# Kernel tuning notes

Hardware: AMD Instinct MI355X
Metric: run time of the kernel (lower is better)

## Reference

```python
import jax, jax.numpy as jnp
import numpy as np

NHEAD = 8
STRIP = 7  # strip_width (horizontal strips, is_vertical=False)


def setup_inputs() -> dict:
    key = jax.random.key(0)
    k0, k1, k2 = jax.random.split(key, 3)
    B, H, W, C = 2, 112, 112, 256
    x = jax.random.normal(k0, (B, H * W, C), dtype=jnp.float32)
    # torch nn.Linear weights: (out_features, in_features)
    qkv_w = jax.random.normal(k1, (3 * C, C), dtype=jnp.float32) * 0.02
    proj_w = jax.random.normal(k2, (C, C), dtype=jnp.float32) * 0.02
    proj_b = jnp.zeros((C,), dtype=jnp.float32)
    return {"x": x, "qkv_w": qkv_w, "proj_w": proj_w, "proj_b": proj_b,
            "H_feat": 112, "W_feat": 112}


def reference(x, qkv_w, proj_w, proj_b, H_feat, W_feat):
    B, N, C = x.shape
    hd = C // NHEAD
    scale = hd ** -0.5
    n_strips = H_feat // STRIP
    L = STRIP * W_feat  # tokens per horizontal strip
    # window_partition with window (STRIP, W_feat): nwW==1, so a pure reshape
    xs = x.reshape(B * n_strips, L, C)
    # qkv projection (Linear: y = x @ W^T), then split q/k/v and heads
    qkv = jnp.einsum('bnc,dc->bnd', xs, qkv_w)
    qkv = qkv.reshape(B * n_strips, L, 3, NHEAD, hd)
    q, k, v = jnp.moveaxis(qkv, 2, 0)  # each (Bw, L, H, hd)
    attn = jnp.einsum('bnhd,bmhd->bhnm', q * scale, k)
    attn = jax.nn.softmax(attn, axis=-1)
    out = jnp.einsum('bhnm,bmhd->bnhd', attn, v).reshape(B * n_strips, L, C)
    out = jnp.einsum('bnc,dc->bnd', out, proj_w) + proj_b
    # window_reverse is again a pure reshape for horizontal strips
    return out.reshape(B, N, C)
```

## Files before the change

kernel.cpp:

```cpp
#include <hip/hip_runtime.h>
#include <hip/hip_bf16.h>

#define M_ROWS 25088
#define CDIM   256
#define QKVD   768
#define LWIN   784
#define NWINH  256

typedef __attribute__((ext_vector_type(8))) short short8v;
typedef __attribute__((ext_vector_type(4))) float floatx4;

#define CEQ 0.2550660106245232f

static __device__ __forceinline__ float bfs2f(unsigned short s) {
    return __uint_as_float(((unsigned int)s) << 16);
}
static __device__ __forceinline__ unsigned short f2bf(float f) {
    unsigned int x = __float_as_uint(f);
    x += 0x7fffu + ((x >> 16) & 1u);
    return (unsigned short)(x >> 16);
}
static __device__ __forceinline__ unsigned int cvt_pk_bf16(float a, float b) {
    unsigned int r;
    asm("v_cvt_pk_bf16_f32 %0, %1, %2" : "=v"(r) : "v"(a), "v"(b));
    return r;
}
static __device__ __forceinline__ void gld_lds16(const unsigned short* g,
                                                 unsigned short* l) {
    __builtin_amdgcn_global_load_lds(
        (const __attribute__((address_space(1))) unsigned int*)g,
        (__attribute__((address_space(3))) unsigned int*)l, 16, 0, 0);
}

__global__ __launch_bounds__(256) void k_f2bf(
    const float* __restrict__ src, unsigned short* __restrict__ dst, int n8)
{
    const float4* s4 = (const float4*)src;
    uint4* d4 = (uint4*)dst;
    for (int i = blockIdx.x * 256 + threadIdx.x; i < n8;
         i += gridDim.x * 256) {
        float4 a = s4[2 * i], b = s4[2 * i + 1];
        uint4 o;
        o.x = cvt_pk_bf16(a.x, a.y);
        o.y = cvt_pk_bf16(a.z, a.w);
        o.z = cvt_pk_bf16(b.x, b.y);
        o.w = cvt_pk_bf16(b.z, b.w);
        d4[i] = o;
    }
}

template <typename OUT_T, bool BIAS, bool SCALEQ>
__global__ __launch_bounds__(256, 2) void k_gemm_mfma(
    const unsigned short* __restrict__ A,
    const unsigned short* __restrict__ B,
    const float* __restrict__ bias,
    OUT_T* __restrict__ Y, int N)
{
    __shared__ __attribute__((aligned(16))) unsigned short As[128 * 64];
    __shared__ __attribute__((aligned(16))) unsigned short Bs[128 * 64];
    const int t = threadIdx.x;
    const int lane = t & 63, wv = t >> 6;
    const int lq = lane & 15, g = lane >> 4;
    const int wm = wv >> 1, wn = wv & 1;
    const int R0 = blockIdx.y * 128, C0 = blockIdx.x * 128;
    const int lrow = t >> 3, lch = (t & 7) * 8;

    floatx4 acc[4][4];
#pragma unroll
    for (int i = 0; i < 4; ++i)
#pragma unroll
        for (int j = 0; j < 4; ++j) acc[i][j] = (floatx4){0.f, 0.f, 0.f, 0.f};

    for (int kc = 0; kc < 256; kc += 64) {
#pragma unroll
        for (int i = 0; i < 4; ++i) {
            gld_lds16(A + (size_t)(R0 + i * 32 + lrow) * 256 + kc + lch,
                      As + (i * 32 + wv * 8) * 64);
            gld_lds16(B + (size_t)(C0 + i * 32 + lrow) * 256 + kc + lch,
                      Bs + (i * 32 + wv * 8) * 64);
        }
        __syncthreads();
#pragma unroll
        for (int kk = 0; kk < 64; kk += 32) {
            short8v af[4], bf[4];
#pragma unroll
            for (int mi = 0; mi < 4; ++mi)
                af[mi] = *(const short8v*)(As + (wm * 64 + mi * 16 + lq) * 64 +
                                           kk + g * 8);
#pragma unroll
            for (int ni = 0; ni < 4; ++ni)
                bf[ni] = *(const short8v*)(Bs + (wn * 64 + ni * 16 + lq) * 64 +
                                           kk + g * 8);
#pragma unroll
            for (int mi = 0; mi < 4; ++mi)
#pragma unroll
                for (int ni = 0; ni < 4; ++ni)
                    acc[mi][ni] = __builtin_amdgcn_mfma_f32_16x16x32_bf16(
                        af[mi], bf[ni], acc[mi][ni], 0, 0, 0);
        }
        __syncthreads();
    }

#pragma unroll
    for (int mi = 0; mi < 4; ++mi) {
        const size_t rb = (size_t)R0 + wm * 64 + mi * 16 + g * 4;
#pragma unroll
        for (int ni = 0; ni < 4; ++ni) {
            const int col = C0 + wn * 64 + ni * 16 + lq;
            float bv = 0.f;
            if constexpr (BIAS) bv = bias[col];
#pragma unroll
            for (int r = 0; r < 4; ++r) {
                float val = acc[mi][ni][r];
                if constexpr (SCALEQ) { if (col < 256) val *= CEQ; }
                val += bv;
                if constexpr (sizeof(OUT_T) == 2)
                    Y[(rb + r) * N + col] = (OUT_T)f2bf(val);
                else
                    Y[(rb + r) * N + col] = (OUT_T)val;
            }
        }
    }
}

#define VTP32 404
#define KS_SZ (LWIN * 32)
#define VT_SH (2 * 32 * VTP32)
#define PB_OFF (KS_SZ + VT_SH)
#define ATTN_LDS ((PB_OFF + 16 * 1280) * 2)

__global__ __launch_bounds__(1024, 1) void k_attn_mfma(
    const unsigned short* __restrict__ qkv,
    unsigned short* __restrict__ ao)
{
    extern __shared__ unsigned short sm[];
    unsigned short* Ks = sm;
    unsigned int*   Vt = (unsigned int*)(sm + KS_SZ);
    const int t = threadIdx.x;
    const int lane = t & 63, wave = t >> 6;
    const int lq = lane & 15, g = lane >> 4;
    const int h = blockIdx.x & 7, w = blockIdx.x >> 3;
    const size_t rowbase = (size_t)w * LWIN;
    const unsigned short* base = qkv + rowbase * QKVD;

    for (int idx = t; idx < LWIN * 4; idx += 1024) {
        const int row = idx >> 2, c = idx & 3;
        uint4 kv = *(const uint4*)(base + (size_t)row * QKVD + 256 + h * 32 + c * 8);
        *(uint4*)(Ks + c * (LWIN * 8) + row * 8) = kv;
    }
    for (int idx = t; idx < 392 * 4; idx += 1024) {
        const int rp = idx >> 2, c = idx & 3;
        union { uint4 u; unsigned short s[8]; } a, b;
        a.u = *(const uint4*)(base + (size_t)(2 * rp) * QKVD + 512 + h * 32 + c * 8);
        b.u = *(const uint4*)(base + (size_t)(2 * rp + 1) * QKVD + 512 + h * 32 + c * 8);
#pragma unroll
        for (int j = 0; j < 8; ++j)
            Vt[(c * 8 + j) * VTP32 + rp] =
                (unsigned int)a.s[j] | ((unsigned int)b.s[j] << 16);
    }
    for (int idx = t; idx < 32 * 12; idx += 1024) {
        Vt[(idx / 12) * VTP32 + 392 + (idx % 12)] = 0;
    }
    __syncthreads();

    unsigned short* Pw = sm + PB_OFF + wave * 1280;

    for (int tq = wave; tq < 49; tq += 16) {
        const short8v qf = *(const short8v*)(base +
                (size_t)(tq * 16 + lq) * QKVD + h * 32 + g * 8);
        floatx4 oa0 = {0.f, 0.f, 0.f, 0.f}, oa1 = {0.f, 0.f, 0.f, 0.f};
        float lsum = 0.f;

        auto score = [&](int s, int buf) {
            short8v kf = *(const short8v*)(Ks + g * (LWIN * 8) +
                                           (size_t)(s * 16 + lq) * 8);
            floatx4 st = __builtin_amdgcn_mfma_f32_16x16x32_bf16(
                kf, qf, (floatx4){0.f, 0.f, 0.f, 0.f}, 0, 0, 0);
            float p0 = __builtin_amdgcn_exp2f(st[0]);
            float p1 = __builtin_amdgcn_exp2f(st[1]);
            float p2 = __builtin_amdgcn_exp2f(st[2]);
            float p3 = __builtin_amdgcn_exp2f(st[3]);
            lsum += (p0 + p1) + (p2 + p3);
            uint2 pw;
            pw.x = cvt_pk_bf16(p0, p1);
            pw.y = cvt_pk_bf16(p2, p3);
            *(uint2*)(Pw + buf * 640 + lq * 40 + (s & 1) * 16 + g * 4) = pw;
        };
        auto pv = [&](int u) {
            const int woff = u * 16;
            short8v v0 = *(const short8v*)(const unsigned short*)(
                Vt + (size_t)lq * VTP32 + woff + g * 4);
            short8v v1 = *(const short8v*)(const unsigned short*)(
                Vt + (size_t)(lq + 16) * VTP32 + woff + g * 4);
            short8v pf = *(const short8v*)(Pw + (u & 1) * 640 + lq * 40 + g * 8);
            oa0 = __builtin_amdgcn_mfma_f32_16x16x32_bf16(pf, v0, oa0, 0, 0, 0);
            oa1 = __builtin_amdgcn_mfma_f32_16x16x32_bf16(pf, v1, oa1, 0, 0, 0);
        };

        score(0, 0);
        score(1, 0);
        for (int u = 1; u < 24; ++u) {
            score(2 * u, u & 1);
            pv(u - 1);
            score(2 * u + 1, u & 1);
        }
        score(48, 0);
        pv(23);
        {
            uint2 z; z.x = 0u; z.y = 0u;
            *(uint2*)(Pw + lq * 40 + 16 + g * 4) = z;
        }
        pv(24);

        float l = lsum;
        l += __shfl_xor(l, 16);
        l += __shfl_xor(l, 32);
        float inv = 1.f / l;
        const size_t orow0 = rowbase + (size_t)tq * 16;
#pragma unroll
        for (int r = 0; r < 4; ++r) {
            float ir = __shfl(inv, (lane & 48) | (g * 4 + r));
            size_t ob = (orow0 + g * 4 + r) * CDIM + h * 32;
            ao[ob + lq]      = f2bf(oa0[r] * ir);
            ao[ob + 16 + lq] = f2bf(oa1[r] * ir);
        }
    }
}

extern "C" void kernel_launch(void* const* d_in, const int* in_sizes, int n_in,
                              void* d_out, int out_size, void* d_ws, size_t ws_size,
                              hipStream_t stream) {
    const float* x      = (const float*)d_in[0];
    const float* qkv_w  = (const float*)d_in[1];
    const float* proj_w = (const float*)d_in[2];
    const float* proj_b = (const float*)d_in[3];
    float* out = (float*)d_out;

    unsigned short* qkvb = (unsigned short*)d_ws;
    unsigned short* xb   = qkvb + (size_t)M_ROWS * QKVD;
    unsigned short* aob  = xb;
    unsigned short* wqb  = xb + (size_t)M_ROWS * CDIM;
    unsigned short* wpb  = wqb + (size_t)QKVD * CDIM;

    hipFuncSetAttribute((const void*)k_attn_mfma,
                        hipFuncAttributeMaxDynamicSharedMemorySize, ATTN_LDS);

    k_f2bf<<<2048, 256, 0, stream>>>(x, xb, (M_ROWS * CDIM) / 8);
    k_f2bf<<<96, 256, 0, stream>>>(qkv_w, wqb, (QKVD * CDIM) / 8);
    k_f2bf<<<32, 256, 0, stream>>>(proj_w, wpb, (CDIM * CDIM) / 8);

    k_gemm_mfma<unsigned short, false, true>
        <<<dim3(QKVD / 128, M_ROWS / 128), 256, 0, stream>>>(
            xb, wqb, nullptr, qkvb, QKVD);

    k_attn_mfma<<<dim3(NWINH), 1024, ATTN_LDS, stream>>>(qkvb, aob);

    k_gemm_mfma<float, true, false>
        <<<dim3(CDIM / 128, M_ROWS / 128), 256, 0, stream>>>(
            aob, wpb, proj_b, out, CDIM);
}
```

Before: 90.35 us.

## Keep P in registers and process multiple query tiles per wave in attention

Each wave now handles 3–4 query tiles at once, so every K fragment and V fragment loaded from LDS is reused across several score and PV MFMAs. The V transpose is permuted at load time so that the score MFMA output layout feeds the PV MFMA A-operand directly, which removes the per-wave P staging buffer in LDS. K is stored row-major with a padded pitch. This trades more registers per wave for less LDS traffic, at the cost of load imbalance: wave 0 does 4 tiles while the rest do 3.

Result: faster. 88.12 us (-2.5%).

```diff
diff --git a/kernel.cpp b/kernel.cpp
--- a/kernel.cpp
+++ b/kernel.cpp
@@ -12,9 +12,6 @@
 
 #define CEQ 0.2550660106245232f
 
-static __device__ __forceinline__ float bfs2f(unsigned short s) {
-    return __uint_as_float(((unsigned int)s) << 16);
-}
 static __device__ __forceinline__ unsigned short f2bf(float f) {
     unsigned int x = __float_as_uint(f);
     x += 0x7fffu + ((x >> 16) & 1u);
@@ -123,11 +120,10 @@
     }
 }
 
-#define VTP32 404
-#define KS_SZ (LWIN * 32)
-#define VT_SH (2 * 32 * VTP32)
-#define PB_OFF (KS_SZ + VT_SH)
-#define ATTN_LDS ((PB_OFF + 16 * 1280) * 2)
+#define KPITCH 36
+#define VPITCH 404
+#define KS_SZ  (LWIN * KPITCH)
+#define ATTN_LDS (KS_SZ * 2 + 32 * VPITCH * 4)
 
 __global__ __launch_bounds__(1024, 1) void k_attn_mfma(
     const unsigned short* __restrict__ qkv,
@@ -146,83 +142,111 @@
     for (int idx = t; idx < LWIN * 4; idx += 1024) {
         const int row = idx >> 2, c = idx & 3;
         uint4 kv = *(const uint4*)(base + (size_t)row * QKVD + 256 + h * 32 + c * 8);
-        *(uint4*)(Ks + c * (LWIN * 8) + row * 8) = kv;
-    }
-    for (int idx = t; idx < 392 * 4; idx += 1024) {
-        const int rp = idx >> 2, c = idx & 3;
-        union { uint4 u; unsigned short s[8]; } a, b;
-        a.u = *(const uint4*)(base + (size_t)(2 * rp) * QKVD + 512 + h * 32 + c * 8);
-        b.u = *(const uint4*)(base + (size_t)(2 * rp + 1) * QKVD + 512 + h * 32 + c * 8);
-#pragma unroll
-        for (int j = 0; j < 8; ++j)
-            Vt[(c * 8 + j) * VTP32 + rp] =
-                (unsigned int)a.s[j] | ((unsigned int)b.s[j] << 16);
-    }
-    for (int idx = t; idx < 32 * 12; idx += 1024) {
-        Vt[(idx / 12) * VTP32 + 392 + (idx % 12)] = 0;
+        *(uint4*)(Ks + row * KPITCH + c * 8) = kv;
+    }
+    {
+        const int c = t >> 8;
+        const int p0 = t & 255;
+        for (int tp = p0; tp < 392; tp += 256) {
+            const int u = tp >> 4, tpp = tp & 15;
+            const int a = tpp >> 3, gg = (tpp >> 1) & 3, rp = tpp & 1;
+            const int wrd = u * 16 + gg * 4 + a * 2 + rp;
+            union { uint4 u4; unsigned short s[8]; } x0, x1;
+            x0.u4 = *(const uint4*)(base + (size_t)(2 * tp) * QKVD + 512 + h * 32 + c * 8);
+            x1.u4 = *(const uint4*)(base + (size_t)(2 * tp + 1) * QKVD + 512 + h * 32 + c * 8);
+#pragma unroll
+            for (int j = 0; j < 8; ++j)
+                Vt[(c * 8 + j) * VPITCH + wrd] =
+                    (unsigned int)x0.s[j] | ((unsigned int)x1.s[j] << 16);
+        }
+    }
+    for (int idx = t; idx < 32 * 8; idx += 1024) {
+        const int d = idx >> 3, q = idx & 7;
+        Vt[d * VPITCH + 384 + (q >> 1) * 4 + 2 + (q & 1)] = 0;
     }
     __syncthreads();
 
-    unsigned short* Pw = sm + PB_OFF + wave * 1280;
-
-    for (int tq = wave; tq < 49; tq += 16) {
-        const short8v qf = *(const short8v*)(base +
-                (size_t)(tq * 16 + lq) * QKVD + h * 32 + g * 8);
-        floatx4 oa0 = {0.f, 0.f, 0.f, 0.f}, oa1 = {0.f, 0.f, 0.f, 0.f};
-        float lsum = 0.f;
-
-        auto score = [&](int s, int buf) {
-            short8v kf = *(const short8v*)(Ks + g * (LWIN * 8) +
-                                           (size_t)(s * 16 + lq) * 8);
-            floatx4 st = __builtin_amdgcn_mfma_f32_16x16x32_bf16(
-                kf, qf, (floatx4){0.f, 0.f, 0.f, 0.f}, 0, 0, 0);
-            float p0 = __builtin_amdgcn_exp2f(st[0]);
-            float p1 = __builtin_amdgcn_exp2f(st[1]);
-            float p2 = __builtin_amdgcn_exp2f(st[2]);
-            float p3 = __builtin_amdgcn_exp2f(st[3]);
-            lsum += (p0 + p1) + (p2 + p3);
-            uint2 pw;
-            pw.x = cvt_pk_bf16(p0, p1);
-            pw.y = cvt_pk_bf16(p2, p3);
-            *(uint2*)(Pw + buf * 640 + lq * 40 + (s & 1) * 16 + g * 4) = pw;
-        };
-        auto pv = [&](int u) {
-            const int woff = u * 16;
-            short8v v0 = *(const short8v*)(const unsigned short*)(
-                Vt + (size_t)lq * VTP32 + woff + g * 4);
-            short8v v1 = *(const short8v*)(const unsigned short*)(
-                Vt + (size_t)(lq + 16) * VTP32 + woff + g * 4);
-            short8v pf = *(const short8v*)(Pw + (u & 1) * 640 + lq * 40 + g * 8);
-            oa0 = __builtin_amdgcn_mfma_f32_16x16x32_bf16(pf, v0, oa0, 0, 0, 0);
-            oa1 = __builtin_amdgcn_mfma_f32_16x16x32_bf16(pf, v1, oa1, 0, 0, 0);
-        };
-
-        score(0, 0);
-        score(1, 0);
-        for (int u = 1; u < 24; ++u) {
-            score(2 * u, u & 1);
-            pv(u - 1);
-            score(2 * u + 1, u & 1);
-        }
-        score(48, 0);
-        pv(23);
+    const int ntile = (wave == 0) ? 4 : 3;
+    const int tbase = (wave == 0) ? 0 : (3 * wave + 1);
+
+    short8v qf[4];
+#pragma unroll
+    for (int n = 0; n < 4; ++n)
+        if (n < ntile)
+            qf[n] = *(const short8v*)(base +
+                    (size_t)((tbase + n) * 16 + lq) * QKVD + h * 32 + g * 8);
+
+    floatx4 oa[4][2];
+#pragma unroll
+    for (int n = 0; n < 4; ++n) {
+        oa[n][0] = (floatx4){0.f, 0.f, 0.f, 0.f};
+        oa[n][1] = (floatx4){0.f, 0.f, 0.f, 0.f};
+    }
+    float lsum[4] = {0.f, 0.f, 0.f, 0.f};
+
+    for (int u = 0; u < 25; ++u) {
+        unsigned int pw[4][4];
         {
-            uint2 z; z.x = 0u; z.y = 0u;
-            *(uint2*)(Pw + lq * 40 + 16 + g * 4) = z;
-        }
-        pv(24);
-
-        float l = lsum;
+            short8v kf = *(const short8v*)(Ks + (size_t)(2 * u * 16 + lq) * KPITCH + g * 8);
+#pragma unroll
+            for (int n = 0; n < 4; ++n) if (n < ntile) {
+                floatx4 st = __builtin_amdgcn_mfma_f32_16x16x32_bf16(
+                    kf, qf[n], (floatx4){0.f, 0.f, 0.f, 0.f}, 0, 0, 0);
+                float p0 = __builtin_amdgcn_exp2f(st[0]);
+                float p1 = __builtin_amdgcn_exp2f(st[1]);
+                float p2 = __builtin_amdgcn_exp2f(st[2]);
+                float p3 = __builtin_amdgcn_exp2f(st[3]);
+                lsum[n] += (p0 + p1) + (p2 + p3);
+                pw[n][0] = cvt_pk_bf16(p0, p1);
+                pw[n][1] = cvt_pk_bf16(p2, p3);
+            }
+        }
+        if (u < 24) {
+            short8v kf = *(const short8v*)(Ks + (size_t)((2 * u + 1) * 16 + lq) * KPITCH + g * 8);
+#pragma unroll
+            for (int n = 0; n < 4; ++n) if (n < ntile) {
+                floatx4 st = __builtin_amdgcn_mfma_f32_16x16x32_bf16(
+                    kf, qf[n], (floatx4){0.f, 0.f, 0.f, 0.f}, 0, 0, 0);
+                float p0 = __builtin_amdgcn_exp2f(st[0]);
+                float p1 = __builtin_amdgcn_exp2f(st[1]);
+                float p2 = __builtin_amdgcn_exp2f(st[2]);
+                float p3 = __builtin_amdgcn_exp2f(st[3]);
+                lsum[n] += (p0 + p1) + (p2 + p3);
+                pw[n][2] = cvt_pk_bf16(p0, p1);
+                pw[n][3] = cvt_pk_bf16(p2, p3);
+            }
+        } else {
+#pragma unroll
+            for (int n = 0; n < 4; ++n) if (n < ntile) {
+                pw[n][2] = 0u; pw[n][3] = 0u;
+            }
+        }
+        const unsigned short* vrow0 = (const unsigned short*)Vt;
+        short8v v0 = *(const short8v*)(vrow0 + (size_t)lq * (VPITCH * 2) + u * 32 + g * 8);
+        short8v v1 = *(const short8v*)(vrow0 + (size_t)(lq + 16) * (VPITCH * 2) + u * 32 + g * 8);
+#pragma unroll
+        for (int n = 0; n < 4; ++n) if (n < ntile) {
+            union { unsigned int wd[4]; short8v v; } pu;
+            pu.wd[0] = pw[n][0]; pu.wd[1] = pw[n][1];
+            pu.wd[2] = pw[n][2]; pu.wd[3] = pw[n][3];
+            oa[n][0] = __builtin_amdgcn_mfma_f32_16x16x32_bf16(pu.v, v0, oa[n][0], 0, 0, 0);
+            oa[n][1] = __builtin_amdgcn_mfma_f32_16x16x32_bf16(pu.v, v1, oa[n][1], 0, 0, 0);
+        }
+    }
+
+#pragma unroll
+    for (int n = 0; n < 4; ++n) if (n < ntile) {
+        float l = lsum[n];
         l += __shfl_xor(l, 16);
         l += __shfl_xor(l, 32);
         float inv = 1.f / l;
-        const size_t orow0 = rowbase + (size_t)tq * 16;
+        const size_t orow0 = rowbase + (size_t)(tbase + n) * 16;
 #pragma unroll
         for (int r = 0; r < 4; ++r) {
             float ir = __shfl(inv, (lane & 48) | (g * 4 + r));
             size_t ob = (orow0 + g * 4 + r) * CDIM + h * 32;
-            ao[ob + lq]      = f2bf(oa0[r] * ir);
-            ao[ob + 16 + lq] = f2bf(oa1[r] * ir);
+            ao[ob + lq]      = f2bf(oa[n][0][r] * ir);
+            ao[ob + 16 + lq] = f2bf(oa[n][1][r] * ir);
         }
     }
 }
```
